# Performance work log

Hardware: AMD Instinct MI355X
Metric: run time of the kernel (lower is better)

Reference implementation:

```python
import jax, jax.numpy as jnp
import numpy as np

B, L, SIZE, ATT, LIN = 8, 2048, 1024, 1024, 4096
EPS = 1e-5


def layer_norm(x, g, b):
    m = x.mean(-1, keepdims=True)
    v = ((x - m) ** 2).mean(-1, keepdims=True)
    return (x - m) * jax.lax.rsqrt(v + EPS) * g + b


def time_shift(x):
    # ZeroPad2d((0,0,1,-1)): prepend a zero timestep, drop the last one
    return jnp.pad(x, ((0, 0), (1, 0), (0, 0)))[:, :-1]


def wkv(time_decay, time_first, k, v):
    """RWKV-v4 WKV linear-attention recurrence (numerically stable, log-space max tracking).
    k, v: (B, L, D). Returns (B, L, D)."""
    w = -jnp.exp(time_decay)  # (D,) per-channel decay (negative)
    u = time_first            # (D,) bonus for current token

    def step(carry, kv):
        p, q, o = carry  # numerator, denominator, running max exponent: (B, D)
        kt, vt = kv      # (B, D)
        no = jnp.maximum(o, u + kt)
        A = jnp.exp(o - no)
        Bc = jnp.exp(u + kt - no)
        out = (A * p + Bc * vt) / (A * q + Bc)
        no2 = jnp.maximum(o + w, kt)
        A2 = jnp.exp(o + w - no2)
        B2 = jnp.exp(kt - no2)
        return (A2 * p + B2 * vt, A2 * q + B2, no2), out

    Bn, Ln, D = k.shape
    init = (jnp.zeros((Bn, D), k.dtype), jnp.zeros((Bn, D), k.dtype),
            jnp.full((Bn, D), -1e38, k.dtype))
    _, out = jax.lax.scan(step, init, (jnp.moveaxis(k, 1, 0), jnp.moveaxis(v, 1, 0)))
    return jnp.moveaxis(out, 0, 1)


def setup_inputs() -> dict:
    key = jax.random.key(0)
    ks = jax.random.split(key, 20)
    n = lambda i, shape, s=1.0: jax.random.normal(ks[i], shape, jnp.float32) * s
    u = lambda i, shape: jax.random.uniform(ks[i], shape, jnp.float32)
    return {
        "x": n(0, (B, L, SIZE)),
        "ln_att_g": jnp.ones((SIZE,), jnp.float32), "ln_att_b": jnp.zeros((SIZE,), jnp.float32),
        "ln_ffn_g": jnp.ones((SIZE,), jnp.float32), "ln_ffn_b": jnp.zeros((SIZE,), jnp.float32),
        "att_time_decay": n(1, (ATT,), 0.5), "att_time_first": n(2, (ATT,), 0.5),
        "att_mix_k": u(3, (SIZE,)), "att_mix_v": u(4, (SIZE,)), "att_mix_r": u(5, (SIZE,)),
        "att_wk": n(6, (SIZE, ATT), 0.02), "att_wv": n(7, (SIZE, ATT), 0.02),
        "att_wr": n(8, (SIZE, ATT), 0.02), "att_wo": n(9, (ATT, SIZE), 0.02),
        "ffn_mix_k": u(10, (SIZE,)), "ffn_mix_r": u(11, (SIZE,)),
        "ffn_wk": n(12, (SIZE, LIN), 0.02), "ffn_wv": n(13, (LIN, SIZE), 0.02),
        "ffn_wr": n(14, (SIZE, SIZE), 0.02),
    }


def reference(x, ln_att_g, ln_att_b, ln_ffn_g, ln_ffn_b,
              att_time_decay, att_time_first, att_mix_k, att_mix_v, att_mix_r,
              att_wk, att_wv, att_wr, att_wo,
              ffn_mix_k, ffn_mix_r, ffn_wk, ffn_wv, ffn_wr):
    # --- time-mixing (WKV attention) branch ---
    h = layer_norm(x, ln_att_g, ln_att_b)
    sx = time_shift(h)
    k = (h * att_mix_k + sx * (1.0 - att_mix_k)) @ att_wk
    v = (h * att_mix_v + sx * (1.0 - att_mix_v)) @ att_wv
    r = jax.nn.sigmoid((h * att_mix_r + sx * (1.0 - att_mix_r)) @ att_wr)
    att = (r * wkv(att_time_decay, att_time_first, k, v)) @ att_wo
    x = x + att  # dropout rate 0.0 (eval)
    # --- channel-mixing (FFN) branch ---
    h = layer_norm(x, ln_ffn_g, ln_ffn_b)
    sx = time_shift(h)
    kf = jnp.square(jax.nn.relu((h * ffn_mix_k + sx * (1.0 - ffn_mix_k)) @ ffn_wk))
    rf = jax.nn.sigmoid((h * ffn_mix_r + sx * (1.0 - ffn_mix_r)) @ ffn_wr)
    return x + rf * (kf @ ffn_wv)
```

## Files before the change

kernel.cpp:

```cpp
#include <hip/hip_runtime.h>
#include <cstdint>
#include <cstddef>

#define BB   8
#define LLEN 2048
#define DSZ  1024
#define FFN  4096
#define MROWS (BB*LLEN)
#define EPSLN 1e-5f
#define WKV_C 32
#define WKV_S (LLEN/WKV_C)
#define WKV_STATES (BB*WKV_C*DSZ)

typedef __bf16 bh8 __attribute__((ext_vector_type(8)));
typedef float  f32x4 __attribute__((ext_vector_type(4)));

__device__ __forceinline__ unsigned short f32_to_bf16(float f) {
  unsigned int u = __float_as_uint(f);
  u += 0x7FFFu + ((u >> 16) & 1u);
  return (unsigned short)(u >> 16);
}
__device__ __forceinline__ float bf16_to_f32(unsigned short u) {
  return __uint_as_float(((unsigned int)u) << 16);
}
__device__ __forceinline__ float bf16_lo(unsigned int u) {
  return __uint_as_float(u << 16);
}
__device__ __forceinline__ float bf16_hi(unsigned int u) {
  return __uint_as_float(u & 0xFFFF0000u);
}
__device__ __forceinline__ unsigned int pack_bf16(float lo, float hi) {
  return (unsigned int)f32_to_bf16(lo) | ((unsigned int)f32_to_bf16(hi) << 16);
}

__device__ __forceinline__ void load_lds16(const void* g, void* l) {
  __builtin_amdgcn_global_load_lds((const __attribute__((address_space(1))) void*)g,
                                   (__attribute__((address_space(3))) void*)l, 16, 0, 0);
}

#define RAW_BAR() asm volatile("s_barrier" ::: "memory")
#define WAIT_VM6() asm volatile("s_waitcnt vmcnt(6)" ::: "memory")
#define WAIT_VM0() asm volatile("s_waitcnt vmcnt(0)" ::: "memory")

__global__ __launch_bounds__(256) void transpose_bf16(const float* __restrict__ W,
                                                      unsigned short* __restrict__ Wt,
                                                      int K, int N) {
  __shared__ float tile[32][33];
  int n0 = blockIdx.x * 32, k0 = blockIdx.y * 32;
  int tx = threadIdx.x, ty = threadIdx.y;
#pragma unroll
  for (int j = 0; j < 32; j += 8)
    tile[ty + j][tx] = W[(size_t)(k0 + ty + j) * N + n0 + tx];
  __syncthreads();
#pragma unroll
  for (int j = 0; j < 32; j += 8)
    Wt[(size_t)(n0 + ty + j) * K + k0 + tx] = f32_to_bf16(tile[tx][ty + j]);
}

__global__ __launch_bounds__(256) void lnmix_att(const float* __restrict__ x,
                                                 const float* __restrict__ g,
                                                 const float* __restrict__ bb,
                                                 const float* __restrict__ mk,
                                                 const float* __restrict__ mv,
                                                 const float* __restrict__ mr,
                                                 unsigned short* __restrict__ xk,
                                                 unsigned short* __restrict__ xv,
                                                 unsigned short* __restrict__ xr) {
  int row = blockIdx.x;
  int t = row & (LLEN - 1);
  int tid = threadIdx.x;
  float4 vc = ((const float4*)(x + (size_t)row * DSZ))[tid];
  float4 vp = make_float4(0.f, 0.f, 0.f, 0.f);
  if (t > 0) vp = ((const float4*)(x + (size_t)(row - 1) * DSZ))[tid];
  float sc = vc.x + vc.y + vc.z + vc.w;
  float qc = vc.x * vc.x + vc.y * vc.y + vc.z * vc.z + vc.w * vc.w;
  float sp = vp.x + vp.y + vp.z + vp.w;
  float qp = vp.x * vp.x + vp.y * vp.y + vp.z * vp.z + vp.w * vp.w;
#pragma unroll
  for (int off = 32; off; off >>= 1) {
    sc += __shfl_down(sc, off); qc += __shfl_down(qc, off);
    sp += __shfl_down(sp, off); qp += __shfl_down(qp, off);
  }
  __shared__ float red[16];
  int lane = tid & 63, w = tid >> 6;
  if (lane == 0) { red[w] = sc; red[4 + w] = qc; red[8 + w] = sp; red[12 + w] = qp; }
  __syncthreads();
  if (tid < 4) red[tid * 4] = red[tid * 4] + red[tid * 4 + 1] + red[tid * 4 + 2] + red[tid * 4 + 3];
  __syncthreads();
  const float invD = 1.f / DSZ;
  float mc = red[0] * invD, rc = rsqrtf(red[4] * invD - mc * mc + EPSLN);
  float mp = red[8] * invD, rp = rsqrtf(red[12] * invD - mp * mp + EPSLN);
  float4 G = ((const float4*)g)[tid], Bv = ((const float4*)bb)[tid];
  float c[4] = { vc.x, vc.y, vc.z, vc.w };
  float p[4] = { vp.x, vp.y, vp.z, vp.w };
  float Ga[4] = { G.x, G.y, G.z, G.w };
  float Ba[4] = { Bv.x, Bv.y, Bv.z, Bv.w };
  float4 K = ((const float4*)mk)[tid];
  float4 V = ((const float4*)mv)[tid];
  float4 R = ((const float4*)mr)[tid];
  float Ka[4] = { K.x, K.y, K.z, K.w };
  float Va[4] = { V.x, V.y, V.z, V.w };
  float Ra[4] = { R.x, R.y, R.z, R.w };
  ushort4 ok, ov, orr;
  unsigned short* okp = &ok.x; unsigned short* ovp = &ov.x; unsigned short* orp = &orr.x;
#pragma unroll
  for (int e = 0; e < 4; ++e) {
    float hc = (c[e] - mc) * rc * Ga[e] + Ba[e];
    float hp = (t > 0) ? (p[e] - mp) * rp * Ga[e] + Ba[e] : 0.f;
    okp[e] = f32_to_bf16(hc * Ka[e] + hp * (1.f - Ka[e]));
    ovp[e] = f32_to_bf16(hc * Va[e] + hp * (1.f - Va[e]));
    orp[e] = f32_to_bf16(hc * Ra[e] + hp * (1.f - Ra[e]));
  }
  size_t e4 = (size_t)row * DSZ + tid * 4;
  *(ushort4*)(xk + e4) = ok;
  *(ushort4*)(xv + e4) = ov;
  *(ushort4*)(xr + e4) = orr;
}

__global__ __launch_bounds__(256) void lnmix_ffn(const float* __restrict__ x,
                                                 const float* __restrict__ g,
                                                 const float* __restrict__ bb,
                                                 const float* __restrict__ mk,
                                                 const float* __restrict__ mr,
                                                 unsigned short* __restrict__ xk,
                                                 unsigned short* __restrict__ xr) {
  int row = blockIdx.x;
  int t = row & (LLEN - 1);
  int tid = threadIdx.x;
  float4 vc = ((const float4*)(x + (size_t)row * DSZ))[tid];
  float4 vp = make_float4(0.f, 0.f, 0.f, 0.f);
  if (t > 0) vp = ((const float4*)(x + (size_t)(row - 1) * DSZ))[tid];
  float sc = vc.x + vc.y + vc.z + vc.w;
  float qc = vc.x * vc.x + vc.y * vc.y + vc.z * vc.z + vc.w * vc.w;
  float sp = vp.x + vp.y + vp.z + vp.w;
  float qp = vp.x * vp.x + vp.y * vp.y + vp.z * vp.z + vp.w * vp.w;
#pragma unroll
  for (int off = 32; off; off >>= 1) {
    sc += __shfl_down(sc, off); qc += __shfl_down(qc, off);
    sp += __shfl_down(sp, off); qp += __shfl_down(qp, off);
  }
  __shared__ float red[16];
  int lane = tid & 63, w = tid >> 6;
  if (lane == 0) { red[w] = sc; red[4 + w] = qc; red[8 + w] = sp; red[12 + w] = qp; }
  __syncthreads();
  if (tid < 4) red[tid * 4] = red[tid * 4] + red[tid * 4 + 1] + red[tid * 4 + 2] + red[tid * 4 + 3];
  __syncthreads();
  const float invD = 1.f / DSZ;
  float mc = red[0] * invD, rc = rsqrtf(red[4] * invD - mc * mc + EPSLN);
  float mp = red[8] * invD, rp = rsqrtf(red[12] * invD - mp * mp + EPSLN);
  float4 G = ((const float4*)g)[tid], Bv = ((const float4*)bb)[tid];
  float c[4] = { vc.x, vc.y, vc.z, vc.w };
  float p[4] = { vp.x, vp.y, vp.z, vp.w };
  float Ga[4] = { G.x, G.y, G.z, G.w };
  float Ba[4] = { Bv.x, Bv.y, Bv.z, Bv.w };
  float4 K = ((const float4*)mk)[tid];
  float4 R = ((const float4*)mr)[tid];
  float Ka[4] = { K.x, K.y, K.z, K.w };
  float Ra[4] = { R.x, R.y, R.z, R.w };
  ushort4 ok, orr;
  unsigned short* okp = &ok.x; unsigned short* orp = &orr.x;
#pragma unroll
  for (int e = 0; e < 4; ++e) {
    float hc = (c[e] - mc) * rc * Ga[e] + Ba[e];
    float hp = (t > 0) ? (p[e] - mp) * rp * Ga[e] + Ba[e] : 0.f;
    okp[e] = f32_to_bf16(hc * Ka[e] + hp * (1.f - Ka[e]));
    orp[e] = f32_to_bf16(hc * Ra[e] + hp * (1.f - Ra[e]));
  }
  size_t e4 = (size_t)row * DSZ + tid * 4;
  *(ushort4*)(xk + e4) = ok;
  *(ushort4*)(xr + e4) = orr;
}

__global__ __launch_bounds__(256) void wkv_pass1(const unsigned int* __restrict__ kk2,
                                                 const unsigned int* __restrict__ vv2,
                                                 const float* __restrict__ td,
                                                 float* __restrict__ sP,
                                                 float* __restrict__ sQ,
                                                 float* __restrict__ sO) {
  int gid = blockIdx.x * 256 + threadIdx.x;
  int d2 = gid & 511;
  int bc = gid >> 9;
  int c  = bc & (WKV_C - 1);
  int b  = bc >> 5;
  int d0 = d2 * 2;
  float w0 = -expf(td[d0]), w1 = -expf(td[d0 + 1]);
  size_t base = ((size_t)b * LLEN + (size_t)c * WKV_S) * 512 + d2;
  float p0 = 0.f, q0 = 0.f, o0 = -1e38f;
  float p1 = 0.f, q1 = 0.f, o1 = -1e38f;
  unsigned int kc = kk2[base], vc = vv2[base];
  unsigned int kA = 0, vA = 0, kB = 0, vB = 0;
  if (WKV_S > 1) { kA = kk2[base + 512]; vA = vv2[base + 512]; }
  for (int t = 0; t < WKV_S; ++t) {
    if (t + 2 < WKV_S) {
      size_t nxt = base + (size_t)(t + 2) * 512;
      kB = kk2[nxt]; vB = vv2[nxt];
    } else { kB = 0; vB = 0; }
    {
      float kt = bf16_lo(kc), vt = bf16_lo(vc);
      float ow = o0 + w0;
      float no2 = fmaxf(ow, kt);
      float A2 = expf(ow - no2), B2 = expf(kt - no2);
      p0 = A2 * p0 + B2 * vt; q0 = A2 * q0 + B2; o0 = no2;
    }
    {
      float kt = bf16_hi(kc), vt = bf16_hi(vc);
      float ow = o1 + w1;
      float no2 = fmaxf(ow, kt);
      float A2 = expf(ow - no2), B2 = expf(kt - no2);
      p1 = A2 * p1 + B2 * vt; q1 = A2 * q1 + B2; o1 = no2;
    }
    kc = kA; vc = vA; kA = kB; vA = vB;
  }
  int sidx = (bc << 10) + d0;
  sP[sidx] = p0; sP[sidx + 1] = p1;
  sQ[sidx] = q0; sQ[sidx + 1] = q1;
  sO[sidx] = o0; sO[sidx + 1] = o1;
}

__global__ __launch_bounds__(256) void wkv_combine(const float* __restrict__ sP,
                                                   const float* __restrict__ sQ,
                                                   const float* __restrict__ sO,
                                                   const float* __restrict__ td,
                                                   float* __restrict__ pP,
                                                   float* __restrict__ pQ,
                                                   float* __restrict__ pO) {
  int gid = blockIdx.x * 256 + threadIdx.x;
  int d = gid & (DSZ - 1);
  int b = gid >> 10;
  float w = -expf(td[d]);
  float Sw = (float)WKV_S * w;
  float p = 0.f, q = 0.f, o = -1e38f;
  for (int c = 0; c < WKV_C; ++c) {
    size_t idx = (((size_t)b * WKV_C + c) << 10) + d;
    pP[idx] = p; pQ[idx] = q; pO[idx] = o;
    float lp = sP[idx], lq = sQ[idx], lo = sO[idx];
    float oin = o + Sw;
    float no  = fmaxf(oin, lo);
    float Ai  = expf(oin - no);
    float Al  = expf(lo - no);
    p = Ai * p + Al * lp;
    q = Ai * q + Al * lq;
    o = no;
  }
}

__global__ __launch_bounds__(256) void wkv_pass3(const unsigned int* __restrict__ kk2,
                                                 const unsigned int* __restrict__ vv2,
                                                 const unsigned int* __restrict__ rr2,
                                                 const float* __restrict__ td,
                                                 const float* __restrict__ tf,
                                                 const float* __restrict__ pP,
                                                 const float* __restrict__ pQ,
                                                 const float* __restrict__ pO,
                                                 unsigned int* __restrict__ rw2) {
  int gid = blockIdx.x * 256 + threadIdx.x;
  int d2 = gid & 511;
  int bc = gid >> 9;
  int c  = bc & (WKV_C - 1);
  int b  = bc >> 5;
  int d0 = d2 * 2;
  float w0 = -expf(td[d0]), w1 = -expf(td[d0 + 1]);
  float u0 = tf[d0], u1 = tf[d0 + 1];
  int sidx = (bc << 10) + d0;
  float p0 = pP[sidx], q0 = pQ[sidx], o0 = pO[sidx];
  float p1 = pP[sidx + 1], q1 = pQ[sidx + 1], o1 = pO[sidx + 1];
  size_t base = ((size_t)b * LLEN + (size_t)c * WKV_S) * 512 + d2;
  unsigned int kc = kk2[base], vc = vv2[base], rc = rr2[base];
  unsigned int kA = 0, vA = 0, rA = 0, kB = 0, vB = 0, rB = 0;
  if (WKV_S > 1) { kA = kk2[base + 512]; vA = vv2[base + 512]; rA = rr2[base + 512]; }
  for (int t = 0; t < WKV_S; ++t) {
    if (t + 2 < WKV_S) {
      size_t nxt = base + (size_t)(t + 2) * 512;
      kB = kk2[nxt]; vB = vv2[nxt]; rB = rr2[nxt];
    } else { kB = 0; vB = 0; rB = 0; }
    float out0, out1;
    {
      float kt = bf16_lo(kc), vt = bf16_lo(vc);
      float uk = u0 + kt;
      float no = fmaxf(o0, uk);
      float A  = expf(o0 - no), Bc = expf(uk - no);
      out0 = (A * p0 + Bc * vt) / (A * q0 + Bc);
      float ow = o0 + w0;
      float no2 = fmaxf(ow, kt);
      float A2 = expf(ow - no2), B2 = expf(kt - no2);
      p0 = A2 * p0 + B2 * vt; q0 = A2 * q0 + B2; o0 = no2;
    }
    {
      float kt = bf16_hi(kc), vt = bf16_hi(vc);
      float uk = u1 + kt;
      float no = fmaxf(o1, uk);
      float A  = expf(o1 - no), Bc = expf(uk - no);
      out1 = (A * p1 + Bc * vt) / (A * q1 + Bc);
      float ow = o1 + w1;
      float no2 = fmaxf(ow, kt);
      float A2 = expf(ow - no2), B2 = expf(kt - no2);
      p1 = A2 * p1 + B2 * vt; q1 = A2 * q1 + B2; o1 = no2;
    }
    rw2[base + (size_t)t * 512] = pack_bf16(bf16_lo(rc) * out0, bf16_hi(rc) * out1);
    kc = kA; vc = vA; rc = rA; kA = kB; vA = vB; rA = rB;
  }
}


#define KTILE(T, BUF, BUFN, KO1, KO2)                                             \
  {                                                                               \
           \
    _Pragma("unroll")                                                             \
    for (int mi = 0; mi < 4; ++mi) {                                              \
      a03[mi][0] = *(const bh8*)(smA + (BUF) + aRow + mi * 2048 + sw0);           \
      a03[mi][1] = *(const bh8*)(smA + (BUF) + aRow + mi * 2048 + sw1);           \
    }                                                                             \
    _Pragma("unroll")                                                             \
    for (int nj = 0; nj < 2; ++nj) {                                              \
      b01[nj][0] = *(const bh8*)(smB + (BUF) + bRow + nj * 2048 + sw0);           \
      b01[nj][1] = *(const bh8*)(smB + (BUF) + bRow + nj * 2048 + sw1);           \
    }                                                                             \
    if ((T) + 1 < nk) {                                                           \
      load_lds16(pB1  + (KO1), smB + (BUFN) + 16384 + ldsW);                      \
      load_lds16(pB1b + (KO1), smB + (BUFN) + 16384 + 1024 + ldsW);               \
    }                                                                             \
    RAW_BAR();                                                                    \
    __builtin_amdgcn_s_setprio(1);                                                \
    _Pragma("unroll")                                                             \
    for (int mi = 0; mi < 4; ++mi)                                                \
      _Pragma("unroll")                                                           \
      for (int nj = 0; nj < 2; ++nj) {                                            \
        acc[mi][nj] = __builtin_amdgcn_mfma_f32_16x16x32_bf16(a03[mi][0], b01[nj][0], acc[mi][nj], 0, 0, 0); \
        acc[mi][nj] = __builtin_amdgcn_mfma_f32_16x16x32_bf16(a03[mi][1], b01[nj][1], acc[mi][nj], 0, 0, 0); \
      }                                                                           \
    __builtin_amdgcn_s_setprio(0);                                                \
    RAW_BAR();                                                                    \
                                       \
    _Pragma("unroll")                                                             \
    for (int nj = 0; nj < 2; ++nj) {                                              \
      b23[nj][0] = *(const bh8*)(smB + (BUF) + bRow + (nj + 2) * 2048 + sw0);     \
      b23[nj][1] = *(const bh8*)(smB + (BUF) + bRow + (nj + 2) * 2048 + sw1);     \
    }                                                                             \
    RAW_BAR();                                                                    \
    __builtin_amdgcn_s_setprio(1);                                                \
    _Pragma("unroll")                                                             \
    for (int mi = 0; mi < 4; ++mi)                                                \
      _Pragma("unroll")                                                           \
      for (int nj = 0; nj < 2; ++nj) {                                            \
        acc[mi][nj + 2] = __builtin_amdgcn_mfma_f32_16x16x32_bf16(a03[mi][0], b23[nj][0], acc[mi][nj + 2], 0, 0, 0); \
        acc[mi][nj + 2] = __builtin_amdgcn_mfma_f32_16x16x32_bf16(a03[mi][1], b23[nj][1], acc[mi][nj + 2], 0, 0, 0); \
      }                                                                           \
    __builtin_amdgcn_s_setprio(0);                                                \
    RAW_BAR();                                                                    \
                 \
    _Pragma("unroll")                                                             \
    for (int mi = 0; mi < 4; ++mi) {                                              \
      a47[mi][0] = *(const bh8*)(smA + (BUF) + aRow + (mi + 4) * 2048 + sw0);     \
      a47[mi][1] = *(const bh8*)(smA + (BUF) + aRow + (mi + 4) * 2048 + sw1);     \
    }                                                                             \
    if ((T) + 2 < nk) {                                                           \
      load_lds16(pB0  + (KO2), smB + (BUF) + ldsW);                               \
      load_lds16(pB0b + (KO2), smB + (BUF) + 1024 + ldsW);                        \
    }                                                                             \
    RAW_BAR();                                                                    \
    __builtin_amdgcn_s_setprio(1);                                                \
    _Pragma("unroll")                                                             \
    for (int mi = 0; mi < 4; ++mi)                                                \
      _Pragma("unroll")                                                           \
      for (int nj = 0; nj < 2; ++nj) {                                            \
        acc[mi + 4][nj] = __builtin_amdgcn_mfma_f32_16x16x32_bf16(a47[mi][0], b01[nj][0], acc[mi + 4][nj], 0, 0, 0); \
        acc[mi + 4][nj] = __builtin_amdgcn_mfma_f32_16x16x32_bf16(a47[mi][1], b01[nj][1], acc[mi + 4][nj], 0, 0, 0); \
      }                                                                           \
    __builtin_amdgcn_s_setprio(0);                                                \
    RAW_BAR();                                                                    \
         \
    if ((T) + 2 < nk) {                                                           \
      load_lds16(pA0  + (KO2), smA + (BUF) + ldsW);                               \
      load_lds16(pA0b + (KO2), smA + (BUF) + 1024 + ldsW);                        \
      load_lds16(pA1  + (KO2), smA + (BUF) + 16384 + ldsW);                       \
      load_lds16(pA1b + (KO2), smA + (BUF) + 16384 + 1024 + ldsW);                \
    }                                                                             \
    RAW_BAR();                                                                    \
    __builtin_amdgcn_s_setprio(1);                                                \
    _Pragma("unroll")                                                             \
    for (int mi = 0; mi < 4; ++mi)                                                \
      _Pragma("unroll")                                                           \
      for (int nj = 0; nj < 2; ++nj) {                                            \
        acc[mi + 4][nj + 2] = __builtin_amdgcn_mfma_f32_16x16x32_bf16(a47[mi][0], b23[nj][0], acc[mi + 4][nj + 2], 0, 0, 0); \
        acc[mi + 4][nj + 2] = __builtin_amdgcn_mfma_f32_16x16x32_bf16(a47[mi][1], b23[nj][1], acc[mi + 4][nj + 2], 0, 0, 0); \
      }                                                                           \
    __builtin_amdgcn_s_setprio(0);                                                \
    if ((T) + 2 < nk) { WAIT_VM6(); } else { WAIT_VM0(); }                        \
    RAW_BAR();                                                                    \
  }

template <int EPI>
__global__ __launch_bounds__(512, 2) void gemm256(const unsigned short* __restrict__ A,
                                                  const unsigned short* __restrict__ Bt,
                                                  float* __restrict__ C,
                                                  unsigned short* __restrict__ Cbf,
                                                  const float* __restrict__ aux1,
                                                  const unsigned short* __restrict__ aux2b,
                                                  int M, int N, int K) {
  extern __shared__ unsigned char sm[];
  unsigned char* smA = sm;
  unsigned char* smB = sm + 65536;

  const int tid  = threadIdx.x;
  const int lane = tid & 63;
  const int wid  = tid >> 6;
  const int wr   = wid >> 2;
  const int wc   = wid & 3;

  int nwg = gridDim.x;
  int gx  = N >> 8;
  int wg  = blockIdx.x;
  int swzid = ((nwg & 7) == 0) ? ((wg & 7) * (nwg >> 3) + (wg >> 3)) : wg;
  int bn = swzid % gx, bm = swzid / gx;

  const unsigned short* Ab = A  + (size_t)bm * 256 * K;
  const unsigned short* Bb = Bt + (size_t)bn * 256 * K;

  const int nk = K >> 6;

  const int r15 = lane & 15;
  const int sw0 = ((((lane >> 4)    ) ^ (lane & 7)) << 4);
  const int sw1 = (((4 | (lane >> 4)) ^ (lane & 7)) << 4);
  const int aRow = wr * 16384 + r15 * 128;
  const int bRow = wc * 8192  + r15 * 128;
  const int ldsW = wid * 2048 + lane * 16;

  const int grow = lane >> 3;
  const int colS = (((lane & 7) ^ grow) << 3);
  const unsigned short* pA0  = Ab + (size_t)(wid * 16 + grow) * K + colS;
  const unsigned short* pA0b = pA0 + (size_t)8 * K;
  const unsigned short* pA1  = pA0 + (size_t)128 * K;
  const unsigned short* pA1b = pA1 + (size_t)8 * K;
  const unsigned short* pB0  = Bb + (size_t)(wid * 16 + grow) * K + colS;
  const unsigned short* pB0b = pB0 + (size_t)8 * K;
  const unsigned short* pB1  = pB0 + (size_t)128 * K;
  const unsigned short* pB1b = pB1 + (size_t)8 * K;

  f32x4 acc[8][4];
#pragma unroll
  for (int i = 0; i < 8; ++i)
#pragma unroll
    for (int j = 0; j < 4; ++j)
#pragma unroll
      for (int e = 0; e < 4; ++e) acc[i][j][e] = 0.f;

  load_lds16(pA0,       smA + ldsW);
  load_lds16(pA0b,      smA + 1024 + ldsW);
  load_lds16(pA1,       smA + 16384 + ldsW);
  load_lds16(pA1b,      smA + 16384 + 1024 + ldsW);
  load_lds16(pB0,       smB + ldsW);
  load_lds16(pB0b,      smB + 1024 + ldsW);
  load_lds16(pB1,       smB + 16384 + ldsW);
  load_lds16(pB1b,      smB + 16384 + 1024 + ldsW);
  load_lds16(pB0 + 64,  smB + 32768 + ldsW);
  load_lds16(pB0b + 64, smB + 32768 + 1024 + ldsW);
  load_lds16(pA0 + 64,  smA + 32768 + ldsW);
  load_lds16(pA0b + 64, smA + 32768 + 1024 + ldsW);
  load_lds16(pA1 + 64,  smA + 32768 + 16384 + ldsW);
  load_lds16(pA1b + 64, smA + 32768 + 16384 + 1024 + ldsW);
  WAIT_VM6();
  RAW_BAR();

  bh8 a03[4][2], a47[4][2], b01[2][2], b23[2][2];

  for (int tb = 0; tb < nk; tb += 2) {
    KTILE(tb,     0,     32768, 64,  128);
    KTILE(tb + 1, 32768, 0,     128, 192);
    pA0 += 128; pA0b += 128; pA1 += 128; pA1b += 128;
    pB0 += 128; pB0b += 128; pB1 += 128; pB1b += 128;
  }

  const int r4 = (lane >> 4) * 4, cn = lane & 15;
#pragma unroll
  for (int mi = 0; mi < 8; ++mi) {
#pragma unroll
    for (int nj = 0; nj < 4; ++nj) {
      int col = bn * 256 + wc * 64 + nj * 16 + cn;
#pragma unroll
      for (int e = 0; e < 4; ++e) {
        int row = bm * 256 + wr * 128 + mi * 16 + r4 + e;
        size_t idx = (size_t)row * N + col;
        float val = acc[mi][nj][e];
        if (EPI == 0) {
          Cbf[idx] = f32_to_bf16(val);
        } else if (EPI == 1) {
          Cbf[idx] = f32_to_bf16(1.f / (1.f + expf(-val)));
        } else if (EPI == 2) {
          C[idx] = aux1[idx] + val;
        } else if (EPI == 3) {
          float tt = val > 0.f ? val : 0.f;
          Cbf[idx] = f32_to_bf16(tt * tt);
        } else {
          C[idx] = aux1[idx] + bf16_to_f32(aux2b[idx]) * val;
        }
      }
    }
  }
}

extern "C" void kernel_launch(void* const* d_in, const int* in_sizes, int n_in,
                              void* d_out, int out_size, void* d_ws, size_t ws_size,
                              hipStream_t stream) {
  const float* x        = (const float*)d_in[0];
  const float* ln_att_g = (const float*)d_in[1];
  const float* ln_att_b = (const float*)d_in[2];
  const float* ln_ffn_g = (const float*)d_in[3];
  const float* ln_ffn_b = (const float*)d_in[4];
  const float* td       = (const float*)d_in[5];
  const float* tf       = (const float*)d_in[6];
  const float* amk      = (const float*)d_in[7];
  const float* amv      = (const float*)d_in[8];
  const float* amr      = (const float*)d_in[9];
  const float* att_wk   = (const float*)d_in[10];
  const float* att_wv   = (const float*)d_in[11];
  const float* att_wr   = (const float*)d_in[12];
  const float* att_wo   = (const float*)d_in[13];
  const float* fmk      = (const float*)d_in[14];
  const float* fmr      = (const float*)d_in[15];
  const float* ffn_wk   = (const float*)d_in[16];
  const float* ffn_wv   = (const float*)d_in[17];
  const float* ffn_wr   = (const float*)d_in[18];
  float* out = (float*)d_out;
  (void)in_sizes; (void)n_in; (void)out_size;

  const size_t WBYTES  = 4 * ((size_t)DSZ * DSZ * 2)
                       + (size_t)FFN * DSZ * 2
                       + (size_t)DSZ * FFN * 2
                       + (size_t)DSZ * DSZ * 2;
  const size_t BUF     = (size_t)MROWS * DSZ * 2;
  const size_t NEEDED  = WBYTES + 4 * BUF + 2 * BUF;
  if (ws_size < NEEDED) return;

  char* ws = (char*)d_ws;
  size_t off = 0;
  auto take = [&](size_t bytes) { char* p = ws + off; off += (bytes + 255) & ~(size_t)255; return p; };

  unsigned short* wkT  = (unsigned short*)take((size_t)DSZ * DSZ * 2);
  unsigned short* wvT  = (unsigned short*)take((size_t)DSZ * DSZ * 2);
  unsigned short* wrT  = (unsigned short*)take((size_t)DSZ * DSZ * 2);
  unsigned short* woT  = (unsigned short*)take((size_t)DSZ * DSZ * 2);
  unsigned short* fwkT = (unsigned short*)take((size_t)FFN * DSZ * 2);
  unsigned short* fwvT = (unsigned short*)take((size_t)DSZ * FFN * 2);
  unsigned short* fwrT = (unsigned short*)take((size_t)DSZ * DSZ * 2);
  unsigned short* bufA = (unsigned short*)take(BUF);
  unsigned short* bufB = (unsigned short*)take(BUF);
  unsigned short* bufC = (unsigned short*)take(BUF);
  unsigned short* bufD = (unsigned short*)take(BUF);
  char*           eReg = take(2 * BUF);
  unsigned short* kf = bufC;

  float* sP = (float*)eReg;
  float* sQ = sP + WKV_STATES;
  float* sO = sQ + WKV_STATES;
  float* pP = sO + WKV_STATES;
  float* pQ = pP + WKV_STATES;
  float* pO = pQ + WKV_STATES;

  dim3 tb(32, 8);
  transpose_bf16<<<dim3(DSZ / 32, DSZ / 32), tb, 0, stream>>>(att_wk, wkT, DSZ, DSZ);
  transpose_bf16<<<dim3(DSZ / 32, DSZ / 32), tb, 0, stream>>>(att_wv, wvT, DSZ, DSZ);
  transpose_bf16<<<dim3(DSZ / 32, DSZ / 32), tb, 0, stream>>>(att_wr, wrT, DSZ, DSZ);
  transpose_bf16<<<dim3(DSZ / 32, DSZ / 32), tb, 0, stream>>>(att_wo, woT, DSZ, DSZ);
  transpose_bf16<<<dim3(FFN / 32, DSZ / 32), tb, 0, stream>>>(ffn_wk, fwkT, DSZ, FFN);
  transpose_bf16<<<dim3(DSZ / 32, FFN / 32), tb, 0, stream>>>(ffn_wv, fwvT, FFN, DSZ);
  transpose_bf16<<<dim3(DSZ / 32, DSZ / 32), tb, 0, stream>>>(ffn_wr, fwrT, DSZ, DSZ);

  const int LDSB = 131072;
  const int G1   = (MROWS / 256) * (DSZ / 256);
  const int G2   = (MROWS / 256) * (FFN / 256);

  lnmix_att<<<MROWS, 256, 0, stream>>>(x, ln_att_g, ln_att_b, amk, amv, amr, bufA, bufB, bufC);
  gemm256<0><<<G1, 512, LDSB, stream>>>(bufA, wkT, nullptr, bufD, nullptr, nullptr, MROWS, DSZ, DSZ);
  gemm256<0><<<G1, 512, LDSB, stream>>>(bufB, wvT, nullptr, bufA, nullptr, nullptr, MROWS, DSZ, DSZ);
  gemm256<1><<<G1, 512, LDSB, stream>>>(bufC, wrT, nullptr, bufB, nullptr, nullptr, MROWS, DSZ, DSZ);
  wkv_pass1<<<(WKV_STATES / 2) / 256, 256, 0, stream>>>((const unsigned int*)bufD, (const unsigned int*)bufA, td, sP, sQ, sO);
  wkv_combine<<<(BB * DSZ) / 256, 256, 0, stream>>>(sP, sQ, sO, td, pP, pQ, pO);
  wkv_pass3<<<(WKV_STATES / 2) / 256, 256, 0, stream>>>((const unsigned int*)bufD, (const unsigned int*)bufA, (const unsigned int*)bufB, td, tf, pP, pQ, pO, (unsigned int*)bufC);
  gemm256<2><<<G1, 512, LDSB, stream>>>(bufC, woT, out, nullptr, x, nullptr, MROWS, DSZ, DSZ);

  lnmix_ffn<<<MROWS, 256, 0, stream>>>(out, ln_ffn_g, ln_ffn_b, fmk, fmr, bufA, bufB);
  gemm256<3><<<G2, 512, LDSB, stream>>>(bufA, fwkT, nullptr, kf, nullptr, nullptr, MROWS, FFN, DSZ);
  gemm256<1><<<G1, 512, LDSB, stream>>>(bufB, fwrT, nullptr, bufA, nullptr, nullptr, MROWS, DSZ, DSZ);
  gemm256<4><<<G1, 512, LDSB, stream>>>(kf, fwvT, out, nullptr, out, bufA, MROWS, DSZ, FFN);
}
```

Before: 689.0 us.

## Batch K/V/R projection GEMMs into one launch and double WKV chunk count

Merges the three separate key/value/receptance projection GEMMs into a single grouped kernel whose grid covers all three, with sigmoid applied only for the receptance group. This removes two launches and the tail under-utilisation of each small GEMM. The WKV chunked scan also moves from 32 to 64 chunks per sequence, giving more parallel threads for the pass1/pass3 recurrences at the cost of a larger state buffer and combine work. Workspace buffers are reshuffled so the bigger state arrays and the new v/r outputs fit.

```diff
diff --git a/kernel.cpp b/kernel.cpp
--- a/kernel.cpp
+++ b/kernel.cpp
@@ -8,7 +8,7 @@
 #define FFN  4096
 #define MROWS (BB*LLEN)
 #define EPSLN 1e-5f
-#define WKV_C 32
+#define WKV_C 64
 #define WKV_S (LLEN/WKV_C)
 #define WKV_STATES (BB*WKV_C*DSZ)
 
@@ -181,7 +181,7 @@
   int d2 = gid & 511;
   int bc = gid >> 9;
   int c  = bc & (WKV_C - 1);
-  int b  = bc >> 5;
+  int b  = bc >> 6;
   int d0 = d2 * 2;
   float w0 = -expf(td[d0]), w1 = -expf(td[d0 + 1]);
   size_t base = ((size_t)b * LLEN + (size_t)c * WKV_S) * 512 + d2;
@@ -257,7 +257,7 @@
   int d2 = gid & 511;
   int bc = gid >> 9;
   int c  = bc & (WKV_C - 1);
-  int b  = bc >> 5;
+  int b  = bc >> 6;
   int d0 = d2 * 2;
   float w0 = -expf(td[d0]), w1 = -expf(td[d0 + 1]);
   float u0 = tf[d0], u1 = tf[d0 + 1];
@@ -301,10 +301,8 @@
   }
 }
 
-
 #define KTILE(T, BUF, BUFN, KO1, KO2)                                             \
   {                                                                               \
-           \
     _Pragma("unroll")                                                             \
     for (int mi = 0; mi < 4; ++mi) {                                              \
       a03[mi][0] = *(const bh8*)(smA + (BUF) + aRow + mi * 2048 + sw0);           \
@@ -330,7 +328,6 @@
       }                                                                           \
     __builtin_amdgcn_s_setprio(0);                                                \
     RAW_BAR();                                                                    \
-                                       \
     _Pragma("unroll")                                                             \
     for (int nj = 0; nj < 2; ++nj) {                                              \
       b23[nj][0] = *(const bh8*)(smB + (BUF) + bRow + (nj + 2) * 2048 + sw0);     \
@@ -347,7 +344,6 @@
       }                                                                           \
     __builtin_amdgcn_s_setprio(0);                                                \
     RAW_BAR();                                                                    \
-                 \
     _Pragma("unroll")                                                             \
     for (int mi = 0; mi < 4; ++mi) {                                              \
       a47[mi][0] = *(const bh8*)(smA + (BUF) + aRow + (mi + 4) * 2048 + sw0);     \
@@ -368,7 +364,6 @@
       }                                                                           \
     __builtin_amdgcn_s_setprio(0);                                                \
     RAW_BAR();                                                                    \
-         \
     if ((T) + 2 < nk) {                                                           \
       load_lds16(pA0  + (KO2), smA + (BUF) + ldsW);                               \
       load_lds16(pA0b + (KO2), smA + (BUF) + 1024 + ldsW);                        \
@@ -387,6 +382,57 @@
     __builtin_amdgcn_s_setprio(0);                                                \
     if ((T) + 2 < nk) { WAIT_VM6(); } else { WAIT_VM0(); }                        \
     RAW_BAR();                                                                    \
+  }
+
+#define GEMM_SETUP(AB, BB_, KD)                                                   \
+  const unsigned short* Ab = (AB);                                                \
+  const unsigned short* Bb = (BB_);                                               \
+  const int nk = (KD) >> 6;                                                       \
+  const int r15 = lane & 15;                                                      \
+  const int sw0 = ((((lane >> 4)    ) ^ (lane & 7)) << 4);                        \
+  const int sw1 = (((4 | (lane >> 4)) ^ (lane & 7)) << 4);                        \
+  const int aRow = wr * 16384 + r15 * 128;                                        \
+  const int bRow = wc * 8192  + r15 * 128;                                        \
+  const int ldsW = wid * 2048 + lane * 16;                                        \
+  const int grow = lane >> 3;                                                     \
+  const int colS = (((lane & 7) ^ grow) << 3);                                    \
+  const unsigned short* pA0  = Ab + (size_t)(wid * 16 + grow) * (KD) + colS;      \
+  const unsigned short* pA0b = pA0 + (size_t)8 * (KD);                            \
+  const unsigned short* pA1  = pA0 + (size_t)128 * (KD);                          \
+  const unsigned short* pA1b = pA1 + (size_t)8 * (KD);                            \
+  const unsigned short* pB0  = Bb + (size_t)(wid * 16 + grow) * (KD) + colS;      \
+  const unsigned short* pB0b = pB0 + (size_t)8 * (KD);                            \
+  const unsigned short* pB1  = pB0 + (size_t)128 * (KD);                          \
+  const unsigned short* pB1b = pB1 + (size_t)8 * (KD);                            \
+  f32x4 acc[8][4];                                                                \
+  _Pragma("unroll")                                                               \
+  for (int i = 0; i < 8; ++i)                                                     \
+    _Pragma("unroll")                                                             \
+    for (int j = 0; j < 4; ++j)                                                   \
+      _Pragma("unroll")                                                           \
+      for (int e = 0; e < 4; ++e) acc[i][j][e] = 0.f;                             \
+  load_lds16(pA0,       smA + ldsW);                                              \
+  load_lds16(pA0b,      smA + 1024 + ldsW);                                       \
+  load_lds16(pA1,       smA + 16384 + ldsW);                                      \
+  load_lds16(pA1b,      smA + 16384 + 1024 + ldsW);                               \
+  load_lds16(pB0,       smB + ldsW);                                              \
+  load_lds16(pB0b,      smB + 1024 + ldsW);                                       \
+  load_lds16(pB1,       smB + 16384 + ldsW);                                      \
+  load_lds16(pB1b,      smB + 16384 + 1024 + ldsW);                               \
+  load_lds16(pB0 + 64,  smB + 32768 + ldsW);                                      \
+  load_lds16(pB0b + 64, smB + 32768 + 1024 + ldsW);                               \
+  load_lds16(pA0 + 64,  smA + 32768 + ldsW);                                      \
+  load_lds16(pA0b + 64, smA + 32768 + 1024 + ldsW);                               \
+  load_lds16(pA1 + 64,  smA + 32768 + 16384 + ldsW);                              \
+  load_lds16(pA1b + 64, smA + 32768 + 16384 + 1024 + ldsW);                       \
+  WAIT_VM6();                                                                     \
+  RAW_BAR();                                                                      \
+  bh8 a03[4][2], a47[4][2], b01[2][2], b23[2][2];                                 \
+  for (int tb = 0; tb < nk; tb += 2) {                                            \
+    KTILE(tb,     0,     32768, 64,  128);                                        \
+    KTILE(tb + 1, 32768, 0,     128, 192);                                        \
+    pA0 += 128; pA0b += 128; pA1 += 128; pA1b += 128;                             \
+    pB0 += 128; pB0b += 128; pB1 += 128; pB1b += 128;                             \
   }
 
 template <int EPI>
@@ -400,75 +446,18 @@
   extern __shared__ unsigned char sm[];
   unsigned char* smA = sm;
   unsigned char* smB = sm + 65536;
-
   const int tid  = threadIdx.x;
   const int lane = tid & 63;
   const int wid  = tid >> 6;
   const int wr   = wid >> 2;
   const int wc   = wid & 3;
-
   int nwg = gridDim.x;
   int gx  = N >> 8;
   int wg  = blockIdx.x;
   int swzid = ((nwg & 7) == 0) ? ((wg & 7) * (nwg >> 3) + (wg >> 3)) : wg;
   int bn = swzid % gx, bm = swzid / gx;
 
-  const unsigned short* Ab = A  + (size_t)bm * 256 * K;
-  const unsigned short* Bb = Bt + (size_t)bn * 256 * K;
-
-  const int nk = K >> 6;
-
-  const int r15 = lane & 15;
-  const int sw0 = ((((lane >> 4)    ) ^ (lane & 7)) << 4);
-  const int sw1 = (((4 | (lane >> 4)) ^ (lane & 7)) << 4);
-  const int aRow = wr * 16384 + r15 * 128;
-  const int bRow = wc * 8192  + r15 * 128;
-  const int ldsW = wid * 2048 + lane * 16;
-
-  const int grow = lane >> 3;
-  const int colS = (((lane & 7) ^ grow) << 3);
-  const unsigned short* pA0  = Ab + (size_t)(wid * 16 + grow) * K + colS;
-  const unsigned short* pA0b = pA0 + (size_t)8 * K;
-  const unsigned short* pA1  = pA0 + (size_t)128 * K;
-  const unsigned short* pA1b = pA1 + (size_t)8 * K;
-  const unsigned short* pB0  = Bb + (size_t)(wid * 16 + grow) * K + colS;
-  const unsigned short* pB0b = pB0 + (size_t)8 * K;
-  const unsigned short* pB1  = pB0 + (size_t)128 * K;
-  const unsigned short* pB1b = pB1 + (size_t)8 * K;
-
-  f32x4 acc[8][4];
-#pragma unroll
-  for (int i = 0; i < 8; ++i)
-#pragma unroll
-    for (int j = 0; j < 4; ++j)
-#pragma unroll
-      for (int e = 0; e < 4; ++e) acc[i][j][e] = 0.f;
-
-  load_lds16(pA0,       smA + ldsW);
-  load_lds16(pA0b,      smA + 1024 + ldsW);
-  load_lds16(pA1,       smA + 16384 + ldsW);
-  load_lds16(pA1b,      smA + 16384 + 1024 + ldsW);
-  load_lds16(pB0,       smB + ldsW);
-  load_lds16(pB0b,      smB + 1024 + ldsW);
-  load_lds16(pB1,       smB + 16384 + ldsW);
-  load_lds16(pB1b,      smB + 16384 + 1024 + ldsW);
-  load_lds16(pB0 + 64,  smB + 32768 + ldsW);
-  load_lds16(pB0b + 64, smB + 32768 + 1024 + ldsW);
-  load_lds16(pA0 + 64,  smA + 32768 + ldsW);
-  load_lds16(pA0b + 64, smA + 32768 + 1024 + ldsW);
-  load_lds16(pA1 + 64,  smA + 32768 + 16384 + ldsW);
-  load_lds16(pA1b + 64, smA + 32768 + 16384 + 1024 + ldsW);
-  WAIT_VM6();
-  RAW_BAR();
-
-  bh8 a03[4][2], a47[4][2], b01[2][2], b23[2][2];
-
-  for (int tb = 0; tb < nk; tb += 2) {
-    KTILE(tb,     0,     32768, 64,  128);
-    KTILE(tb + 1, 32768, 0,     128, 192);
-    pA0 += 128; pA0b += 128; pA1 += 128; pA1b += 128;
-    pB0 += 128; pB0b += 128; pB1 += 128; pB1b += 128;
-  }
+  GEMM_SETUP(A + (size_t)bm * 256 * K, Bt + (size_t)bn * 256 * K, K)
 
   const int r4 = (lane >> 4) * 4, cn = lane & 15;
 #pragma unroll
@@ -493,6 +482,54 @@
         } else {
           C[idx] = aux1[idx] + bf16_to_f32(aux2b[idx]) * val;
         }
+      }
+    }
+  }
+}
+
+__global__ __launch_bounds__(512, 2) void gemm256_kvr(const unsigned short* __restrict__ A0,
+                                                      const unsigned short* __restrict__ A1,
+                                                      const unsigned short* __restrict__ A2,
+                                                      const unsigned short* __restrict__ B0w,
+                                                      const unsigned short* __restrict__ B1w,
+                                                      const unsigned short* __restrict__ B2w,
+                                                      unsigned short* __restrict__ D0,
+                                                      unsigned short* __restrict__ D1,
+                                                      unsigned short* __restrict__ D2) {
+  extern __shared__ unsigned char sm[];
+  unsigned char* smA = sm;
+  unsigned char* smB = sm + 65536;
+  const int tid  = threadIdx.x;
+  const int lane = tid & 63;
+  const int wid  = tid >> 6;
+  const int wr   = wid >> 2;
+  const int wc   = wid & 3;
+  int nwg = gridDim.x;
+  int wg  = blockIdx.x;
+  int swzid = (wg & 7) * (nwg >> 3) + (wg >> 3);
+  int gsel  = swzid >> 8;
+  int local = swzid & 255;
+  int bn = local & 3, bm = local >> 2;
+
+  const unsigned short* Asel = (gsel == 0) ? A0 : (gsel == 1) ? A1 : A2;
+  const unsigned short* Bsel = (gsel == 0) ? B0w : (gsel == 1) ? B1w : B2w;
+  unsigned short*       Dsel = (gsel == 0) ? D0 : (gsel == 1) ? D1 : D2;
+
+  GEMM_SETUP(Asel + (size_t)bm * 256 * DSZ, Bsel + (size_t)bn * 256 * DSZ, DSZ)
+
+  const int r4 = (lane >> 4) * 4, cn = lane & 15;
+  const bool sig = (gsel == 2);
+#pragma unroll
+  for (int mi = 0; mi < 8; ++mi) {
+#pragma unroll
+    for (int nj = 0; nj < 4; ++nj) {
+      int col = bn * 256 + wc * 64 + nj * 16 + cn;
+#pragma unroll
+      for (int e = 0; e < 4; ++e) {
+        int row = bm * 256 + wr * 128 + mi * 16 + r4 + e;
+        size_t idx = (size_t)row * DSZ + col;
+        float val = acc[mi][nj][e];
+        Dsel[idx] = f32_to_bf16(sig ? 1.f / (1.f + expf(-val)) : val);
       }
     }
   }
@@ -548,8 +585,10 @@
   unsigned short* bufD = (unsigned short*)take(BUF);
   char*           eReg = take(2 * BUF);
   unsigned short* kf = bufC;
-
-  float* sP = (float*)eReg;
+  unsigned short* vBuf = (unsigned short*)eReg;
+  unsigned short* rBuf = (unsigned short*)(eReg + BUF);
+
+  float* sP = (float*)bufA;
   float* sQ = sP + WKV_STATES;
   float* sO = sQ + WKV_STATES;
   float* pP = sO + WKV_STATES;
@@ -570,13 +609,11 @@
   const int G2   = (MROWS / 256) * (FFN / 256);
 
   lnmix_att<<<MROWS, 256, 0, stream>>>(x, ln_att_g, ln_att_b, amk, amv, amr, bufA, bufB, bufC);
-  gemm256<0><<<G1, 512, LDSB, stream>>>(bufA, wkT, nullptr, bufD, nullptr, nullptr, MROWS, DSZ, DSZ);
-  gemm256<0><<<G1, 512, LDSB, stream>>>(bufB, wvT, nullptr, bufA, nullptr, nullptr, MROWS, DSZ, DSZ);
-  gemm256<1><<<G1, 512, LDSB, stream>>>(bufC, wrT, nullptr, bufB, nullptr, nullptr, MROWS, DSZ, DSZ);
-  wkv_pass1<<<(WKV_STATES / 2) / 256, 256, 0, stream>>>((const unsigned int*)bufD, (const unsigned int*)bufA, td, sP, sQ, sO);
+  gemm256_kvr<<<3 * G1, 512, LDSB, stream>>>(bufA, bufB, bufC, wkT, wvT, wrT, bufD, vBuf, rBuf);
+  wkv_pass1<<<(WKV_STATES / 2) / 256, 256, 0, stream>>>((const unsigned int*)bufD, (const unsigned int*)vBuf, td, sP, sQ, sO);
   wkv_combine<<<(BB * DSZ) / 256, 256, 0, stream>>>(sP, sQ, sO, td, pP, pQ, pO);
-  wkv_pass3<<<(WKV_STATES / 2) / 256, 256, 0, stream>>>((const unsigned int*)bufD, (const unsigned int*)bufA, (const unsigned int*)bufB, td, tf, pP, pQ, pO, (unsigned int*)bufC);
-  gemm256<2><<<G1, 512, LDSB, stream>>>(bufC, woT, out, nullptr, x, nullptr, MROWS, DSZ, DSZ);
+  wkv_pass3<<<(WKV_STATES / 2) / 256, 256, 0, stream>>>((const unsigned int*)bufD, (const unsigned int*)vBuf, (const unsigned int*)rBuf, td, tf, pP, pQ, pO, (unsigned int*)bufB);
+  gemm256<2><<<G1, 512, LDSB, stream>>>(bufB, woT, out, nullptr, x, nullptr, MROWS, DSZ, DSZ);
 
   lnmix_ffn<<<MROWS, 256, 0, stream>>>(out, ln_ffn_g, ln_ffn_b, fmk, fmr, bufA, bufB);
   gemm256<3><<<G2, 512, LDSB, stream>>>(bufA, fwkT, nullptr, kf, nullptr, nullptr, MROWS, FFN, DSZ);
```

New measurement: 696.3 us. Within noise of the previous version (+1.1%).
